# Performance work log

Measured on AMD Instinct MI355X. Metric: run time of the kernel, lower is better.

The kernel has to match this reference:

```python
import jax, jax.numpy as jnp
import numpy as np

MAX_VAL = 10000.0


def _erode(x, kernel):
    # x: (B, C, H, W); kernel: (kh, kw) flat structuring element (nonzero = active)
    kh, kw = kernel.shape
    oy, ox = kh // 2, kw // 2  # origin = center (rounding toward zero)
    padded = jnp.pad(
        x,
        ((0, 0), (0, 0), (oy, kh - oy - 1), (ox, kw - ox - 1)),
        mode="constant",
        constant_values=MAX_VAL,
    )
    # neighborhood bias: 0 where kernel != 0, -max_val where kernel == 0
    # output[p] = min_k ( padded[p + k] - neighborhood[k] )
    neigh = jnp.where(kernel == 0, -MAX_VAL, 0.0).astype(x.dtype)
    H, W = x.shape[-2], x.shape[-1]
    out = None
    for i in range(kh):  # small fixed k*k loop; no conv/im2col blow-up
        for j in range(kw):
            v = padded[:, :, i:i + H, j:j + W] - neigh[i, j]
            out = v if out is None else jnp.minimum(out, v)
    return out


def setup_inputs() -> dict:
    key = jax.random.key(0)
    x = jax.random.normal(key, (8, 8, 1024, 1024), dtype=jnp.float32)
    kernel = jnp.ones((3, 3), dtype=jnp.float32)
    return {"x": x, "kernel": kernel}


def reference(x, kernel):
    return _erode(x, kernel)
```

## Files before the change

### kernel.cpp

```cpp
#include <hip/hip_runtime.h>

#define MAXV 10000.0f

typedef float fx4 __attribute__((ext_vector_type(4)));

__device__ __forceinline__ float min3f(float a, float b, float c) {
    return fminf(fminf(a, b), c);
}

template <int R>
__global__ __launch_bounds__(256)
void erode3x3_rows(const float* __restrict__ x,
                   const float* __restrict__ kern,
                   float* __restrict__ out,
                   int H, int W, int segs, int ytiles, int nwg) {
    int bid = blockIdx.x;
    int lb  = bid;
    if ((nwg & 7) == 0) {
        const int cpx = nwg >> 3;
        lb = (bid & 7) * cpx + (bid >> 3);
    }
    long long gid = (long long)lb * blockDim.x + threadIdx.x;
    int seg   = (int)(gid % segs);
    int ytile = (int)((gid / segs) % ytiles);
    long long bc = gid / ((long long)segs * ytiles);

    float nv[3][3];
    bool all_active = true;
#pragma unroll
    for (int i = 0; i < 3; ++i)
#pragma unroll
        for (int j = 0; j < 3; ++j) {
            float kv = kern[i * 3 + j];
            nv[i][j] = (kv == 0.0f) ? -MAXV : 0.0f;
            all_active = all_active && (kv != 0.0f);
        }

    const int y0 = ytile * R;
    const int x0 = seg * 4;
    const float* base  = x   + bc * (long long)H * W;
    float*       obase = out + bc * (long long)H * W;

    if (all_active) {
        fx4 ha = MAXV, hb = MAXV, hc = MAXV;
#pragma unroll
        for (int r = 0; r < R + 2; ++r) {
            const int ry = y0 - 1 + r;
            fx4 h;
            if (ry >= 0 && ry < H) {
                const float* rp = base + (long long)ry * W + x0;
                const fx4 b = *(const fx4*)rp;
                const float v0 = (seg > 0)        ? rp[-1] : MAXV;
                const float v5 = (seg < segs - 1) ? rp[4]  : MAXV;
                h.x = min3f(v0,  b.x, b.y);
                h.y = min3f(b.x, b.y, b.z);
                h.z = min3f(b.y, b.z, b.w);
                h.w = min3f(b.z, b.w, v5);
            } else {
                h = MAXV;
            }
            ha = hb; hb = hc; hc = h;
            if (r >= 2) {
                fx4 o;
                o.x = min3f(ha.x, hb.x, hc.x);
                o.y = min3f(ha.y, hb.y, hc.y);
                o.z = min3f(ha.z, hb.z, hc.z);
                o.w = min3f(ha.w, hb.w, hc.w);
                *(fx4*)(obase + (long long)(ry - 1) * W + x0) = o;
            }
        }
    } else {
        float a0[6], a1[6], a2[6];
#pragma unroll
        for (int j = 0; j < 6; ++j) { a0[j] = a1[j] = a2[j] = MAXV; }
#pragma unroll
        for (int r = 0; r < R + 2; ++r) {
            const int ry = y0 - 1 + r;
            float cur[6];
            if (ry >= 0 && ry < H) {
                const float* rp = base + (long long)ry * W + x0;
                const fx4 b = *(const fx4*)rp;
                cur[0] = (seg > 0)        ? rp[-1] : MAXV;
                cur[1] = b.x; cur[2] = b.y; cur[3] = b.z; cur[4] = b.w;
                cur[5] = (seg < segs - 1) ? rp[4]  : MAXV;
            } else {
#pragma unroll
                for (int j = 0; j < 6; ++j) cur[j] = MAXV;
            }
#pragma unroll
            for (int j = 0; j < 6; ++j) { a0[j] = a1[j]; a1[j] = a2[j]; a2[j] = cur[j]; }
            if (r >= 2) {
                float o[4];
#pragma unroll
                for (int e = 0; e < 4; ++e) {
                    float m = 3.4e38f;
#pragma unroll
                    for (int j = 0; j < 3; ++j) {
                        m = fminf(m, a0[e + j] - nv[0][j]);
                        m = fminf(m, a1[e + j] - nv[1][j]);
                        m = fminf(m, a2[e + j] - nv[2][j]);
                    }
                    o[e] = m;
                }
                fx4 ov; ov.x = o[0]; ov.y = o[1]; ov.z = o[2]; ov.w = o[3];
                *(fx4*)(obase + (long long)(ry - 1) * W + x0) = ov;
            }
        }
    }
}

extern "C" void kernel_launch(void* const* d_in, const int* in_sizes, int n_in,
                              void* d_out, int out_size, void* d_ws, size_t ws_size,
                              hipStream_t stream) {
    const float* x    = (const float*)d_in[0];
    const float* kern = (const float*)d_in[1];
    float* out        = (float*)d_out;

    const int H = 1024, W = 1024;
    constexpr int R = 16;
    const int segs   = W / 4;
    const int ytiles = H / R;
    const long long BC = (long long)out_size / ((long long)H * W);

    const long long total = BC * (long long)ytiles * segs;
    const int block = 256;
    const long long grid = (total + block - 1) / block;

    erode3x3_rows<R><<<(dim3)(unsigned)grid, block, 0, stream>>>(
        x, kern, out, H, W, segs, ytiles, (int)grid);
}
```

Baseline: 454.6 us.

## Use wavefront shuffles for halo columns, prefetch rows, drop XCD block remap

Neighbouring columns now come from adjacent lanes through __shfl_up/__shfl_down, so only the first and last lane of each wavefront issue an extra scalar load for the halo. Row loads are software-pipelined with a 4-deep register buffer to keep several loads in flight. The XCD-aware block index remapping is removed in favour of plain linear block order. This cuts redundant scalar global loads and exposes more memory-level parallelism, at the cost of more registers and shuffle instructions.

```diff
diff --git a/kernel.cpp b/kernel.cpp
--- a/kernel.cpp
+++ b/kernel.cpp
@@ -13,14 +13,8 @@
 void erode3x3_rows(const float* __restrict__ x,
                    const float* __restrict__ kern,
                    float* __restrict__ out,
-                   int H, int W, int segs, int ytiles, int nwg) {
-    int bid = blockIdx.x;
-    int lb  = bid;
-    if ((nwg & 7) == 0) {
-        const int cpx = nwg >> 3;
-        lb = (bid & 7) * cpx + (bid >> 3);
-    }
-    long long gid = (long long)lb * blockDim.x + threadIdx.x;
+                   int H, int W, int segs, int ytiles) {
+    long long gid = (long long)blockIdx.x * blockDim.x + threadIdx.x;
     int seg   = (int)(gid % segs);
     int ytile = (int)((gid / segs) % ytiles);
     long long bc = gid / ((long long)segs * ytiles);
@@ -42,25 +36,54 @@
     float*       obase = out + bc * (long long)H * W;
 
     if (all_active) {
+        const int lane = threadIdx.x & 63;
+        const bool is_l = (lane == 0);
+        const bool is_r = (lane == 63);
+        const bool has_edge = (is_l && seg > 0) || (is_r && seg + 1 < segs);
+        const int  eoff = is_l ? -1 : 4;
+
+        constexpr int D = 4;
+        fx4  pb[D];
+        float pe[D];
+
+#define ISSUE(r_, s_)                                                      \
+        {                                                                  \
+            const int ry_ = y0 - 1 + (r_);                                 \
+            if (ry_ >= 0 && ry_ < H) {                                     \
+                const float* rp_ = base + (long long)ry_ * W + x0;         \
+                pb[s_] = *(const fx4*)rp_;                                 \
+                pe[s_] = MAXV;                                             \
+                if (has_edge) pe[s_] = rp_[eoff];                          \
+            } else {                                                       \
+                pb[s_] = MAXV;                                             \
+                pe[s_] = MAXV;                                             \
+            }                                                              \
+        }
+
+#pragma unroll
+        for (int r = 0; r < D; ++r) ISSUE(r, r);
+
         fx4 ha = MAXV, hb = MAXV, hc = MAXV;
 #pragma unroll
         for (int r = 0; r < R + 2; ++r) {
-            const int ry = y0 - 1 + r;
+            const fx4  b = pb[r % D];
+            const float e = pe[r % D];
+            if (r + D < R + 2) ISSUE(r + D, r % D);
+
+            float left  = __shfl_up(b.w, 1, 64);
+            float right = __shfl_down(b.x, 1, 64);
+            left  = is_l ? e : left;
+            right = is_r ? e : right;
+
             fx4 h;
-            if (ry >= 0 && ry < H) {
-                const float* rp = base + (long long)ry * W + x0;
-                const fx4 b = *(const fx4*)rp;
-                const float v0 = (seg > 0)        ? rp[-1] : MAXV;
-                const float v5 = (seg < segs - 1) ? rp[4]  : MAXV;
-                h.x = min3f(v0,  b.x, b.y);
-                h.y = min3f(b.x, b.y, b.z);
-                h.z = min3f(b.y, b.z, b.w);
-                h.w = min3f(b.z, b.w, v5);
-            } else {
-                h = MAXV;
-            }
+            h.x = min3f(left, b.x, b.y);
+            h.y = min3f(b.x,  b.y, b.z);
+            h.z = min3f(b.y,  b.z, b.w);
+            h.w = min3f(b.z,  b.w, right);
+
             ha = hb; hb = hc; hc = h;
             if (r >= 2) {
+                const int ry = y0 - 1 + r;
                 fx4 o;
                 o.x = min3f(ha.x, hb.x, hc.x);
                 o.y = min3f(ha.y, hb.y, hc.y);
@@ -69,6 +92,7 @@
                 *(fx4*)(obase + (long long)(ry - 1) * W + x0) = o;
             }
         }
+#undef ISSUE
     } else {
         float a0[6], a1[6], a2[6];
 #pragma unroll
@@ -127,5 +151,5 @@
     const long long grid = (total + block - 1) / block;
 
     erode3x3_rows<R><<<(dim3)(unsigned)grid, block, 0, stream>>>(
-        x, kern, out, H, W, segs, ytiles, (int)grid);
+        x, kern, out, H, W, segs, ytiles);
 }
```

After: 439.5 us. 3.3% less time.
